# Kernel tuning notes

Measured on AMD Instinct MI355X. Metric: run time of the kernel, lower is better.

The kernel has to match this reference:

```python
import jax, jax.numpy as jnp
import numpy as np


def setup_inputs() -> dict:
    key = jax.random.key(0)
    k1, k2, k3 = jax.random.split(key, 3)
    B, S, D, E, H = 4, 2048, 1024, 8, 1024
    x = jax.random.normal(k1, (B, S, D), dtype=jnp.float32)
    Wg = jax.random.normal(k2, (D, E), dtype=jnp.float32) / np.sqrt(D)
    We = jax.random.normal(k3, (E, D, H), dtype=jnp.float32) / np.sqrt(D)
    be = jnp.zeros((E, H), dtype=jnp.float32)
    return {"x": x, "Wg": Wg, "We": We, "be": be}


def reference(x, Wg, We, be):
    B, S, D = x.shape
    E = Wg.shape[1]
    T = B * S
    xf = x.reshape(T, D)
    # Top-2 gating (softmax over experts, renormalize the chosen 2)
    gates = jax.nn.softmax(xf @ Wg, axis=-1)                 # [T, E]
    top_g, top_i = jax.lax.top_k(gates, 2)                   # [T, 2]
    top_g = top_g / jnp.sum(top_g, axis=-1, keepdims=True)
    # Dense dispatch matrix: dispatch[e, t] = combined gate weight of token t for expert e
    tok = jnp.arange(T)
    dispatch = jnp.zeros((E, T), dtype=gates.dtype)
    for i in range(2):  # fixed top-2, not a data loop
        dispatch = dispatch.at[top_i[:, i], tok].add(top_g[:, i])
    # Per-expert linear (grouped GEMM over all tokens), then weighted combine
    y = jnp.einsum('td,edh->eth', xf, We) + be[:, None, :]   # [E, T, H]
    out = jnp.einsum('et,eth->th', dispatch, y)              # [T, H]
    return out.reshape(B, S, -1)
```

## Files before the change

kernel.cpp:

```cpp
#include <hip/hip_runtime.h>
#include <hip/hip_bf16.h>

#define T_TOK 8192
#define DDIM  1024
#define NEXP  8
#define HDIM  1024
#define SLOT_CAP 17536
#define NCBLK 32

typedef short bf16x8 __attribute__((ext_vector_type(8)));
typedef float f32x4  __attribute__((ext_vector_type(4)));
typedef unsigned short u16x8 __attribute__((ext_vector_type(8)));

typedef const __attribute__((address_space(1))) unsigned int* gas_ptr;
typedef __attribute__((address_space(3))) unsigned int*       las_ptr;
#define GLD16(gp, lp) __builtin_amdgcn_global_load_lds((gas_ptr)(gp), (las_ptr)(lp), 16, 0, 0)

static __device__ __forceinline__ unsigned short f2b(float f) {
    union { float f; unsigned int u; } v; v.f = f;
    unsigned int u = v.u;
    u += 0x7fffu + ((u >> 16) & 1u);
    return (unsigned short)(u >> 16);
}
static __device__ __forceinline__ float b2f(unsigned short h) {
    union { unsigned int u; float f; } v; v.u = ((unsigned int)h) << 16;
    return v.f;
}

__global__ __launch_bounds__(256) void moe_route_wtrans(
    const float* __restrict__ x, const float* __restrict__ wg,
    const float* __restrict__ we,
    unsigned short* __restrict__ xb, unsigned short* __restrict__ wt,
    int* __restrict__ tok_e, float* __restrict__ tok_g)
{
    __shared__ unsigned short tile[64][65];
    int bid = blockIdx.x;
    if (bid < 2048) {
        int wv   = threadIdx.x >> 6;
        int lane = threadIdx.x & 63;
        int t    = bid * 4 + wv;

        const float4* xr = (const float4*)(x + (size_t)t * DDIM);
        float4 v[4];
        #pragma unroll
        for (int i = 0; i < 4; i++) v[i] = xr[lane + 64 * i];

        ushort4* xw = (ushort4*)(xb + (size_t)t * DDIM);
        #pragma unroll
        for (int i = 0; i < 4; i++) {
            ushort4 s4;
            s4.x = f2b(v[i].x); s4.y = f2b(v[i].y);
            s4.z = f2b(v[i].z); s4.w = f2b(v[i].w);
            xw[lane + 64 * i] = s4;
        }

        double s[NEXP];
        #pragma unroll
        for (int e = 0; e < NEXP; e++) s[e] = 0.0;
        #pragma unroll
        for (int i = 0; i < 4; i++) {
            const float* wr = wg + ((size_t)lane * 4 + 256 * i) * NEXP;
            #pragma unroll
            for (int j = 0; j < 4; j++) {
                double xj = (double)((&v[i].x)[j]);
                #pragma unroll
                for (int e = 0; e < NEXP; e++)
                    s[e] += xj * (double)wr[j * NEXP + e];
            }
        }
        #pragma unroll
        for (int off = 32; off > 0; off >>= 1) {
            #pragma unroll
            for (int e = 0; e < NEXP; e++)
                s[e] += __shfl_xor(s[e], off, 64);
        }
        if (lane == 0) {
            int e0 = 0;
            for (int e = 1; e < NEXP; e++) if (s[e] > s[e0]) e0 = e;
            int e1 = (e0 == 0) ? 1 : 0;
            for (int e = 0; e < NEXP; e++) if (e != e0 && s[e] > s[e1]) e1 = e;
            double g0 = 1.0 / (1.0 + exp(s[e1] - s[e0]));
            tok_e[2*t] = e0; tok_e[2*t+1] = e1;
            tok_g[2*t] = (float)g0; tok_g[2*t+1] = (float)(1.0 - g0);
        }
    } else {
        int id = bid - 2048;
        int e  = id >> 8;
        int d0 = ((id >> 4) & 15) * 64;
        int h0 = (id & 15) * 64;
        int c  = threadIdx.x & 63;
        int r4 = threadIdx.x >> 6;
        #pragma unroll
        for (int i = 0; i < 64; i += 4)
            tile[r4 + i][c] = f2b(we[((size_t)e * DDIM + d0 + r4 + i) * HDIM + h0 + c]);
        __syncthreads();
        #pragma unroll
        for (int i = 0; i < 64; i += 4)
            wt[((size_t)e * HDIM + h0 + r4 + i) * DDIM + d0 + c] = tile[c][r4 + i];
    }
}

__global__ __launch_bounds__(256) void moe_count(
    const int* __restrict__ tok_e, int* __restrict__ cnt_part)
{
    __shared__ int h[NEXP];
    if (threadIdx.x < NEXP) h[threadIdx.x] = 0;
    __syncthreads();
    int t = blockIdx.x * 256 + threadIdx.x;
    atomicAdd(&h[tok_e[2*t]], 1);
    atomicAdd(&h[tok_e[2*t+1]], 1);
    __syncthreads();
    if (threadIdx.x < NEXP)
        cnt_part[blockIdx.x * NEXP + threadIdx.x] = h[threadIdx.x];
}

__global__ __launch_bounds__(256) void moe_slotfill(
    const int* __restrict__ tok_e, const int* __restrict__ cnt_part,
    int* __restrict__ meta, int* __restrict__ counts,
    int* __restrict__ slot_token, int* __restrict__ tok_slot)
{
    __shared__ int h[NEXP];
    __shared__ int tots[NEXP], pres[NEXP], base[NEXP];
    int tid = threadIdx.x;
    if (tid < NEXP) h[tid] = 0;
    __syncthreads();
    int t = blockIdx.x * 256 + tid;
    int e0 = tok_e[2*t],     e1 = tok_e[2*t + 1];
    int r0 = atomicAdd(&h[e0], 1);
    int r1 = atomicAdd(&h[e1], 1);
    if (tid < NEXP) {
        int pre = 0, tot = 0;
        for (int b = 0; b < NCBLK; b++) {
            int c = cnt_part[b * NEXP + tid];
            if (b < (int)blockIdx.x) pre += c;
            tot += c;
        }
        tots[tid] = tot; pres[tid] = pre;
    }
    __syncthreads();
    if (tid < NEXP) {
        int off = 0;
        for (int e = 0; e < tid; e++) off += (tots[e] + 127) & ~127;
        base[tid] = off + pres[tid];
        if (blockIdx.x == 0) {
            meta[tid]   = off;
            counts[tid] = tots[tid];
            if (tid == NEXP - 1) meta[NEXP] = off + ((tots[tid] + 127) & ~127);
        }
    }
    __syncthreads();
    int s0 = base[e0] + r0, s1 = base[e1] + r1;
    slot_token[s0] = t;  tok_slot[2*t]     = s0;
    slot_token[s1] = t;  tok_slot[2*t + 1] = s1;
}

__global__ __launch_bounds__(256, 3) void moe_gemm(
    const unsigned short* __restrict__ xb,
    const unsigned short* __restrict__ wt,
    const float* __restrict__ be,
    const int* __restrict__ slot_token,
    const int* __restrict__ meta,
    const int* __restrict__ counts,
    unsigned short* __restrict__ y_slot)
{
    __shared__ __align__(16) unsigned short As[3][128 * 32];
    __shared__ __align__(16) unsigned short Bs[3][128 * 32];

    int f   = blockIdx.y * gridDim.x + blockIdx.x;
    int wid = (f & 7) * gridDim.y + (f >> 3);
    int m0 = (wid >> 3) * 128;
    if (m0 >= meta[NEXP]) return;
    int n0 = (wid & 7) * 128;

    int e = 0;
    #pragma unroll
    for (int i = 1; i < NEXP; i++) if (m0 >= meta[i]) e = i;
    int lim = meta[e] + counts[e];

    int tid  = threadIdx.x;
    int lane = tid & 63, wv = tid >> 6;

    int rA = 32 * wv + (lane >> 2);
    int kc = (((lane & 3) ^ ((rA >> 1) & 3)) * 8);
    int sA0 = m0 + rA, sA1 = sA0 + 16;
    int tA0 = (sA0 < lim) ? slot_token[sA0] : 0;
    int tA1 = (sA1 < lim) ? slot_token[sA1] : 0;
    const unsigned short* gA0 = xb + (size_t)tA0 * DDIM + kc;
    const unsigned short* gA1 = xb + (size_t)tA1 * DDIM + kc;
    const unsigned short* gB0 = wt + ((size_t)e * HDIM + n0 + rA) * DDIM + kc;
    const unsigned short* gB1 = gB0 + (size_t)16 * DDIM;
    int c0 = (2 * wv) * 512;
    int c1 = c0 + 512;

    f32x4 acc[4][4];
    #pragma unroll
    for (int i = 0; i < 4; i++)
        #pragma unroll
        for (int j = 0; j < 4; j++) acc[i][j] = (f32x4){0.f, 0.f, 0.f, 0.f};

    int wm = (wv >> 1) * 64, wn = (wv & 1) * 64;
    int l16 = lane & 15, quad = lane >> 4;
    int ff = (l16 >> 1) & 3;
    int rdA[4], rdB[4];
    #pragma unroll
    for (int i = 0; i < 4; i++) {
        rdA[i] = (wm + i * 16 + l16) * 32 + ((quad ^ ff) * 8);
        rdB[i] = (wn + i * 16 + l16) * 32 + ((quad ^ ff) * 8);
    }

#define ISSUE_A(kkv, Ab)                                                      \
    {                                                                         \
        int ko = (kkv) * 32;                                                  \
        GLD16(gA0 + ko, (Ab) + c0);                                           \
        GLD16(gA1 + ko, (Ab) + c1);                                           \
    }
#define ISSUE_B(kkv, Bb)                                                      \
    {                                                                         \
        int ko = (kkv) * 32;                                                  \
        GLD16(gB0 + ko, (Bb) + c0);                                           \
        GLD16(gB1 + ko, (Bb) + c1);                                           \
    }
#define COMPUTE(Ab, Bb)                                                       \
    {                                                                         \
        bf16x8 bfr[4];                                                        \
        _Pragma("unroll")                                                     \
        for (int j = 0; j < 4; j++)                                           \
            bfr[j] = *(const bf16x8*)((Bb) + rdB[j]);                         \
        _Pragma("unroll")                                                     \
        for (int i = 0; i < 4; i++) {                                         \
            bf16x8 af = *(const bf16x8*)((Ab) + rdA[i]);                      \
            _Pragma("unroll")                                                 \
            for (int j = 0; j < 4; j++)                                       \
                acc[i][j] = __builtin_amdgcn_mfma_f32_16x16x32_bf16(          \
                    af, bfr[j], acc[i][j], 0, 0, 0);                          \
        }                                                                     \
    }

    unsigned short *A0 = As[0], *A1 = As[1], *A2 = As[2];
    unsigned short *B0 = Bs[0], *B1 = Bs[1], *B2 = Bs[2];

    ISSUE_A(0, A0)
    ISSUE_B(0, B0)
    ISSUE_A(1, A1)
    ISSUE_B(1, B1)

    #pragma unroll 1
    for (int kk = 0; kk < 32; ++kk) {
        asm volatile("" ::: "memory");
        if (kk == 31) __builtin_amdgcn_s_waitcnt(0x0F70);
        else          __builtin_amdgcn_s_waitcnt(0x0F74);
        __builtin_amdgcn_s_barrier();
        asm volatile("" ::: "memory");
        if (kk < 30) {
            ISSUE_B(kk + 2, B2)
            ISSUE_A(kk + 2, A2)
        }
        COMPUTE(A0, B0)
        unsigned short* tA = A0; A0 = A1; A1 = A2; A2 = tA;
        unsigned short* tB = B0; B0 = B1; B1 = tB; tB = B1;
        B1 = B2; B2 = tB;
    }
#undef ISSUE_A
#undef ISSUE_B
#undef COMPUTE

    #pragma unroll
    for (int i = 0; i < 4; i++) {
        #pragma unroll
        for (int r = 0; r < 4; r++) {
            int slot = m0 + wm + i * 16 + quad * 4 + r;
            if (slot >= lim) continue;
            unsigned short* yp = y_slot + (size_t)slot * HDIM + n0;
            #pragma unroll
            for (int j = 0; j < 4; j++) {
                int col = wn + j * 16 + l16;
                yp[col] = f2b(acc[i][j][r] + be[e * HDIM + n0 + col]);
            }
        }
    }
}

__global__ __launch_bounds__(256) void moe_combine(
    const unsigned short* __restrict__ y_slot,
    const int* __restrict__ tok_slot, const float* __restrict__ tok_g,
    float* __restrict__ out)
{
    int tid  = threadIdx.x;
    int half = tid >> 7;
    int lane = tid & 127;
    int t = blockIdx.x * 2 + half;
    int s0 = tok_slot[2 * t], s1 = tok_slot[2 * t + 1];
    float g0 = tok_g[2 * t],  g1 = tok_g[2 * t + 1];
    u16x8 a = ((const u16x8*)(y_slot + (size_t)s0 * HDIM))[lane];
    u16x8 b = ((const u16x8*)(y_slot + (size_t)s1 * HDIM))[lane];
    float4 o0, o1;
    o0.x = g0 * b2f(a[0]) + g1 * b2f(b[0]);
    o0.y = g0 * b2f(a[1]) + g1 * b2f(b[1]);
    o0.z = g0 * b2f(a[2]) + g1 * b2f(b[2]);
    o0.w = g0 * b2f(a[3]) + g1 * b2f(b[3]);
    o1.x = g0 * b2f(a[4]) + g1 * b2f(b[4]);
    o1.y = g0 * b2f(a[5]) + g1 * b2f(b[5]);
    o1.z = g0 * b2f(a[6]) + g1 * b2f(b[6]);
    o1.w = g0 * b2f(a[7]) + g1 * b2f(b[7]);
    float4* op = (float4*)(out + (size_t)t * HDIM) + lane * 2;
    op[0] = o0;
    op[1] = o1;
}

extern "C" void kernel_launch(void* const* d_in, const int* in_sizes, int n_in,
                              void* d_out, int out_size, void* d_ws, size_t ws_size,
                              hipStream_t stream) {
    const float* x  = (const float*)d_in[0];
    const float* wg = (const float*)d_in[1];
    const float* we = (const float*)d_in[2];
    const float* be = (const float*)d_in[3];
    float* out = (float*)d_out;

    char* ws = (char*)d_ws;
    size_t o = 0;
    auto alloc = [&](size_t bytes) -> void* {
        void* p = ws + o;
        o = (o + bytes + 255) & ~(size_t)255;
        return p;
    };
    unsigned short* xb   = (unsigned short*)alloc((size_t)T_TOK * DDIM * 2);
    unsigned short* wtb  = (unsigned short*)alloc((size_t)NEXP * HDIM * DDIM * 2);
    unsigned short* ysl  = (unsigned short*)alloc((size_t)SLOT_CAP * HDIM * 2);
    int*   slot_token    = (int*)  alloc((size_t)SLOT_CAP * 4);
    int*   cnt_part      = (int*)  alloc((size_t)NCBLK * NEXP * 4);
    int*   counts        = (int*)  alloc(NEXP * 4);
    int*   meta          = (int*)  alloc((NEXP + 1) * 4);
    int*   tok_e         = (int*)  alloc((size_t)T_TOK * 2 * 4);
    float* tok_g         = (float*)alloc((size_t)T_TOK * 2 * 4);
    int*   tok_slot      = (int*)  alloc((size_t)T_TOK * 2 * 4);

    moe_route_wtrans<<<4096, 256, 0, stream>>>(x, wg, we, xb, wtb, tok_e, tok_g);
    moe_count<<<NCBLK, 256, 0, stream>>>(tok_e, cnt_part);
    moe_slotfill<<<NCBLK, 256, 0, stream>>>(tok_e, cnt_part, meta, counts,
                                            slot_token, tok_slot);
    moe_gemm<<<dim3(HDIM / 128, SLOT_CAP / 128), 256, 0, stream>>>(
        xb, wtb, be, slot_token, meta, counts, ysl);
    moe_combine<<<T_TOK / 2, 256, 0, stream>>>(ysl, tok_slot, tok_g, out);
}
```

Baseline: 209.4 us.

## Enlarge MoE GEMM M-tile to 192 with asymmetric A/B buffering and setprio

The grouped GEMM tile grows from 128x128 to 192x128, so each wave computes 6x4 MFMA tiles and each weight load is reused across more token rows. Expert padding and slot capacity now round to multiples of 192 to match. The B operand drops from triple to double buffering, with B prefetched one step ahead and A two steps ahead, and s_setprio is raised around the MFMA block. This cuts weight traffic per FLOP but raises register pressure under launch_bounds(256,3), adds padding waste, and shortens B prefetch lead time.

```diff
diff --git a/kernel.cpp b/kernel.cpp
--- a/kernel.cpp
+++ b/kernel.cpp
@@ -5,7 +5,7 @@
 #define DDIM  1024
 #define NEXP  8
 #define HDIM  1024
-#define SLOT_CAP 17536
+#define SLOT_CAP 18048
 #define NCBLK 32
 
 typedef short bf16x8 __attribute__((ext_vector_type(8)));
@@ -140,12 +140,12 @@
     __syncthreads();
     if (tid < NEXP) {
         int off = 0;
-        for (int e = 0; e < tid; e++) off += (tots[e] + 127) & ~127;
+        for (int e = 0; e < tid; e++) off += ((tots[e] + 191) / 192) * 192;
         base[tid] = off + pres[tid];
         if (blockIdx.x == 0) {
             meta[tid]   = off;
             counts[tid] = tots[tid];
-            if (tid == NEXP - 1) meta[NEXP] = off + ((tots[tid] + 127) & ~127);
+            if (tid == NEXP - 1) meta[NEXP] = off + ((tots[tid] + 191) / 192) * 192;
         }
     }
     __syncthreads();
@@ -163,12 +163,12 @@
     const int* __restrict__ counts,
     unsigned short* __restrict__ y_slot)
 {
-    __shared__ __align__(16) unsigned short As[3][128 * 32];
-    __shared__ __align__(16) unsigned short Bs[3][128 * 32];
+    __shared__ __align__(16) unsigned short As[3][192 * 32];
+    __shared__ __align__(16) unsigned short Bs[2][128 * 32];
 
     int f   = blockIdx.y * gridDim.x + blockIdx.x;
     int wid = (f & 7) * gridDim.y + (f >> 3);
-    int m0 = (wid >> 3) * 128;
+    int m0 = (wid >> 3) * 192;
     if (m0 >= meta[NEXP]) return;
     int n0 = (wid & 7) * 128;
 
@@ -180,45 +180,51 @@
     int tid  = threadIdx.x;
     int lane = tid & 63, wv = tid >> 6;
 
-    int rA = 32 * wv + (lane >> 2);
-    int kc = (((lane & 3) ^ ((rA >> 1) & 3)) * 8);
-    int sA0 = m0 + rA, sA1 = sA0 + 16;
-    int tA0 = (sA0 < lim) ? slot_token[sA0] : 0;
-    int tA1 = (sA1 < lim) ? slot_token[sA1] : 0;
-    const unsigned short* gA0 = xb + (size_t)tA0 * DDIM + kc;
-    const unsigned short* gA1 = xb + (size_t)tA1 * DDIM + kc;
-    const unsigned short* gB0 = wt + ((size_t)e * HDIM + n0 + rA) * DDIM + kc;
-    const unsigned short* gB1 = gB0 + (size_t)16 * DDIM;
-    int c0 = (2 * wv) * 512;
-    int c1 = c0 + 512;
-
-    f32x4 acc[4][4];
-    #pragma unroll
-    for (int i = 0; i < 4; i++)
+    int rr  = lane >> 2;
+    int kc  = (((lane & 3) ^ (((16 * wv + rr) >> 1) & 3)) * 8);
+    int cL[3];
+    #pragma unroll
+    for (int i = 0; i < 3; i++) cL[i] = (wv + 4 * i) * 512;
+
+    int sA[3]; const unsigned short* gA[3];
+    #pragma unroll
+    for (int i = 0; i < 3; i++) {
+        sA[i] = m0 + 16 * (wv + 4 * i) + rr;
+        int tok = (sA[i] < lim) ? slot_token[sA[i]] : 0;
+        gA[i] = xb + (size_t)tok * DDIM + kc;
+    }
+    const unsigned short* gB0 = wt + ((size_t)e * HDIM + n0 + 16 * wv + rr) * DDIM + kc;
+    const unsigned short* gB1 = gB0 + (size_t)64 * DDIM;
+
+    f32x4 acc[6][4];
+    #pragma unroll
+    for (int i = 0; i < 6; i++)
         #pragma unroll
         for (int j = 0; j < 4; j++) acc[i][j] = (f32x4){0.f, 0.f, 0.f, 0.f};
 
-    int wm = (wv >> 1) * 64, wn = (wv & 1) * 64;
+    int wm = (wv >> 1) * 96, wn = (wv & 1) * 64;
     int l16 = lane & 15, quad = lane >> 4;
     int ff = (l16 >> 1) & 3;
-    int rdA[4], rdB[4];
-    #pragma unroll
-    for (int i = 0; i < 4; i++) {
+    int rdA[6], rdB[4];
+    #pragma unroll
+    for (int i = 0; i < 6; i++)
         rdA[i] = (wm + i * 16 + l16) * 32 + ((quad ^ ff) * 8);
-        rdB[i] = (wn + i * 16 + l16) * 32 + ((quad ^ ff) * 8);
-    }
-
-#define ISSUE_A(kkv, Ab)                                                      \
+    #pragma unroll
+    for (int j = 0; j < 4; j++)
+        rdB[j] = (wn + j * 16 + l16) * 32 + ((quad ^ ff) * 8);
+
+#define ISSUE_A(kt, Ab)                                                       \
     {                                                                         \
-        int ko = (kkv) * 32;                                                  \
-        GLD16(gA0 + ko, (Ab) + c0);                                           \
-        GLD16(gA1 + ko, (Ab) + c1);                                           \
-    }
-#define ISSUE_B(kkv, Bb)                                                      \
+        int ko = (kt) * 32;                                                   \
+        GLD16(gA[0] + ko, (Ab) + cL[0]);                                      \
+        GLD16(gA[1] + ko, (Ab) + cL[1]);                                      \
+        GLD16(gA[2] + ko, (Ab) + cL[2]);                                      \
+    }
+#define ISSUE_B(kt, Bb)                                                       \
     {                                                                         \
-        int ko = (kkv) * 32;                                                  \
-        GLD16(gB0 + ko, (Bb) + c0);                                           \
-        GLD16(gB1 + ko, (Bb) + c1);                                           \
+        int ko = (kt) * 32;                                                   \
+        GLD16(gB0 + ko, (Bb) + cL[0]);                                        \
+        GLD16(gB1 + ko, (Bb) + cL[1]);                                        \
     }
 #define COMPUTE(Ab, Bb)                                                       \
     {                                                                         \
@@ -227,7 +233,7 @@
         for (int j = 0; j < 4; j++)                                           \
             bfr[j] = *(const bf16x8*)((Bb) + rdB[j]);                         \
         _Pragma("unroll")                                                     \
-        for (int i = 0; i < 4; i++) {                                         \
+        for (int i = 0; i < 6; i++) {                                         \
             bf16x8 af = *(const bf16x8*)((Ab) + rdA[i]);                      \
             _Pragma("unroll")                                                 \
             for (int j = 0; j < 4; j++)                                       \
@@ -237,35 +243,33 @@
     }
 
     unsigned short *A0 = As[0], *A1 = As[1], *A2 = As[2];
-    unsigned short *B0 = Bs[0], *B1 = Bs[1], *B2 = Bs[2];
+    unsigned short *B0 = Bs[0], *B1 = Bs[1];
 
     ISSUE_A(0, A0)
     ISSUE_B(0, B0)
     ISSUE_A(1, A1)
-    ISSUE_B(1, B1)
 
     #pragma unroll 1
     for (int kk = 0; kk < 32; ++kk) {
         asm volatile("" ::: "memory");
         if (kk == 31) __builtin_amdgcn_s_waitcnt(0x0F70);
-        else          __builtin_amdgcn_s_waitcnt(0x0F74);
+        else          __builtin_amdgcn_s_waitcnt(0x0F73);
         __builtin_amdgcn_s_barrier();
         asm volatile("" ::: "memory");
-        if (kk < 30) {
-            ISSUE_B(kk + 2, B2)
-            ISSUE_A(kk + 2, A2)
-        }
+        if (kk < 31) ISSUE_B(kk + 1, B1)
+        if (kk < 30) ISSUE_A(kk + 2, A2)
+        __builtin_amdgcn_s_setprio(1);
         COMPUTE(A0, B0)
+        __builtin_amdgcn_s_setprio(0);
         unsigned short* tA = A0; A0 = A1; A1 = A2; A2 = tA;
-        unsigned short* tB = B0; B0 = B1; B1 = tB; tB = B1;
-        B1 = B2; B2 = tB;
+        unsigned short* tB = B0; B0 = B1; B1 = tB;
     }
 #undef ISSUE_A
 #undef ISSUE_B
 #undef COMPUTE
 
     #pragma unroll
-    for (int i = 0; i < 4; i++) {
+    for (int i = 0; i < 6; i++) {
         #pragma unroll
         for (int r = 0; r < 4; r++) {
             int slot = m0 + wm + i * 16 + quad * 4 + r;
@@ -338,7 +342,7 @@
     moe_count<<<NCBLK, 256, 0, stream>>>(tok_e, cnt_part);
     moe_slotfill<<<NCBLK, 256, 0, stream>>>(tok_e, cnt_part, meta, counts,
                                             slot_token, tok_slot);
-    moe_gemm<<<dim3(HDIM / 128, SLOT_CAP / 128), 256, 0, stream>>>(
+    moe_gemm<<<dim3(HDIM / 128, SLOT_CAP / 192), 256, 0, stream>>>(
         xb, wtb, be, slot_token, meta, counts, ysl);
     moe_combine<<<T_TOK / 2, 256, 0, stream>>>(ysl, tok_slot, tok_g, out);
 }
```

New measurement: 199.8 us. 1.05x faster.
